# Optimization experiments

Measured on AMD Instinct MI355X. Metric: run time of the kernel, lower is better.

## Reference

```python
import jax, jax.numpy as jnp
import numpy as np

N = 100000   # nodes
K = 32       # fixed neighbor count per node
IN_C = 128
OUT_C = 64


def setup_inputs() -> dict:
    key = jax.random.key(0)
    k1, k2, k3 = jax.random.split(key, 3)
    x = jax.random.normal(k1, (N, IN_C), dtype=jnp.float32)
    nbrs = jax.random.randint(k2, (N, K), 0, N, dtype=jnp.int64)
    # nn.Linear weight [out, in], no bias
    W = jax.random.normal(k3, (OUT_C, IN_C), dtype=jnp.float32) * (1.0 / np.sqrt(IN_C))
    return {"x": x, "nbrs": nbrs, "W": W}


def reference(x, nbrs, W):
    # h = self.w(x): [N, out]
    h = jnp.einsum("ni,oi->no", x, W)
    # gather neighbor features: [N, K, out]
    gathered = h[nbrs]
    # torch.median(dim=0): lower middle element of sorted values (no averaging)
    med_idx = (K - 1) // 2
    out = jnp.sort(gathered, axis=1)[:, med_idx, :]  # [N, out]
    return out
```

## Files before the change

kernel.cpp:

```cpp
#include <hip/hip_runtime.h>
#include <hip/hip_fp16.h>

#define NNODES 100000
#define KNBR 32
#define IN_C 128
#define OUT_C 64

__global__ __launch_bounds__(256) void gemm_h_kernel(
    const float* __restrict__ x, const float* __restrict__ W,
    __half* __restrict__ h)
{
    __shared__ __align__(16) float sx[64 * 68];
    __shared__ __align__(16) float sw[64 * 68];

    const int t = threadIdx.x;
    const int node0 = blockIdx.x * 64;
    const int tx = t & 15;
    const int ty = t >> 4;
    const int kq = t & 15;
    const int sl = t >> 4;

    float acc[4][4];
#pragma unroll
    for (int i = 0; i < 4; ++i)
#pragma unroll
        for (int j = 0; j < 4; ++j) acc[i][j] = 0.f;

    for (int kc = 0; kc < 2; ++kc) {
        const int kbase = kc * 64;
        __syncthreads();
#pragma unroll
        for (int pass = 0; pass < 4; ++pass) {
            const int nl = sl + pass * 16;
            int nn = node0 + nl;
            if (nn > NNODES - 1) nn = NNODES - 1;
            const float4 xv = *(const float4*)(x + nn * IN_C + kbase + 4 * kq);
            sx[(4 * kq + 0) * 68 + nl] = xv.x;
            sx[(4 * kq + 1) * 68 + nl] = xv.y;
            sx[(4 * kq + 2) * 68 + nl] = xv.z;
            sx[(4 * kq + 3) * 68 + nl] = xv.w;
            const float4 wv = *(const float4*)(W + nl * IN_C + kbase + 4 * kq);
            sw[(4 * kq + 0) * 68 + nl] = wv.x;
            sw[(4 * kq + 1) * 68 + nl] = wv.y;
            sw[(4 * kq + 2) * 68 + nl] = wv.z;
            sw[(4 * kq + 3) * 68 + nl] = wv.w;
        }
        __syncthreads();
#pragma unroll 8
        for (int kk = 0; kk < 64; ++kk) {
            const float4 wv = *(const float4*)&sw[kk * 68 + 4 * tx];
            const float4 xv = *(const float4*)&sx[kk * 68 + 4 * ty];
            acc[0][0] += xv.x * wv.x; acc[0][1] += xv.x * wv.y;
            acc[0][2] += xv.x * wv.z; acc[0][3] += xv.x * wv.w;
            acc[1][0] += xv.y * wv.x; acc[1][1] += xv.y * wv.y;
            acc[1][2] += xv.y * wv.z; acc[1][3] += xv.y * wv.w;
            acc[2][0] += xv.z * wv.x; acc[2][1] += xv.z * wv.y;
            acc[2][2] += xv.z * wv.z; acc[2][3] += xv.z * wv.w;
            acc[3][0] += xv.w * wv.x; acc[3][1] += xv.w * wv.y;
            acc[3][2] += xv.w * wv.z; acc[3][3] += xv.w * wv.w;
        }
    }
#pragma unroll
    for (int i = 0; i < 4; ++i) {
        const int node = node0 + 4 * ty + i;
        if (node < NNODES) {
            __half2 p0 = __floats2half2_rn(acc[i][0], acc[i][1]);
            __half2 p1 = __floats2half2_rn(acc[i][2], acc[i][3]);
            uint2 st;
            st.x = *(unsigned int*)&p0;
            st.y = *(unsigned int*)&p1;
            *(uint2*)(h + node * OUT_C + 4 * tx) = st;
        }
    }
}

__device__ __forceinline__ unsigned pk_min(unsigned a, unsigned b) {
    unsigned d;
    asm("v_pk_min_f16 %0, %1, %2" : "=v"(d) : "v"(a), "v"(b));
    return d;
}
__device__ __forceinline__ unsigned pk_max(unsigned a, unsigned b) {
    unsigned d;
    asm("v_pk_max_f16 %0, %1, %2" : "=v"(d) : "v"(a), "v"(b));
    return d;
}
__device__ __forceinline__ void ce(unsigned& a, unsigned& b) {
    const unsigned lo = pk_min(a, b);
    b = pk_max(a, b);
    a = lo;
}

__device__ __forceinline__ void sort16(unsigned* v) {
    constexpr unsigned char net[63][2] = {
        {0,1},{2,3},{4,5},{6,7},{8,9},{10,11},{12,13},{14,15},
        {0,2},{1,3},{4,6},{5,7},{8,10},{9,11},{12,14},{13,15},
        {1,2},{5,6},{9,10},{13,14},
        {0,4},{1,5},{2,6},{3,7},{8,12},{9,13},{10,14},{11,15},
        {2,4},{3,5},{10,12},{11,13},
        {1,2},{3,4},{5,6},{9,10},{11,12},{13,14},
        {0,8},{1,9},{2,10},{3,11},{4,12},{5,13},{6,14},{7,15},
        {4,8},{5,9},{6,10},{7,11},
        {2,4},{3,5},{6,8},{7,9},{10,12},{11,13},
        {1,2},{3,4},{5,6},{7,8},{9,10},{11,12},{13,14}
    };
#pragma unroll
    for (int i = 0; i < 63; ++i) ce(v[net[i][0]], v[net[i][1]]);
}

__device__ __forceinline__ unsigned median32(unsigned* v) {
    sort16(v);
    sort16(v + 16);
    const unsigned* A = v;
    const unsigned* B = v + 16;
    const unsigned e2a = pk_max(pk_max(A[0], B[0]), pk_min(A[8],  B[8]));
    const unsigned o1a = pk_min(pk_max(A[4], B[4]), pk_min(A[12], B[12]));
    const unsigned Ep4 = pk_max(e2a, o1a);
    const unsigned e2b = pk_max(pk_max(A[2], B[2]), pk_min(A[10], B[10]));
    const unsigned o1b = pk_min(pk_max(A[6], B[6]), pk_min(A[14], B[14]));
    const unsigned Op3 = pk_min(e2b, o1b);
    const unsigned E8  = pk_max(Ep4, Op3);
    const unsigned e2c = pk_max(pk_max(A[1], B[1]), pk_min(A[9],  B[9]));
    const unsigned o1c = pk_min(pk_max(A[5], B[5]), pk_min(A[13], B[13]));
    const unsigned Ep4o = pk_max(e2c, o1c);
    const unsigned e2d = pk_max(pk_max(A[3], B[3]), pk_min(A[11], B[11]));
    const unsigned o1d = pk_min(pk_max(A[7], B[7]), pk_min(A[15], B[15]));
    const unsigned Op3o = pk_min(e2d, o1d);
    const unsigned O7  = pk_min(Ep4o, Op3o);
    return pk_min(E8, O7);
}

__global__ __launch_bounds__(256) void median_kernel(
    const __half* __restrict__ h, const int* __restrict__ nbrs,
    float* __restrict__ out)
{
    const int t = threadIdx.x;
    const int li = t & 15;
    const int node = blockIdx.x * 16 + (t >> 4);
    const int ch0 = 4 * li;

    const int ia = nbrs[node * KNBR + li];
    const int ib = nbrs[node * KNBR + 16 + li];

    unsigned a[KNBR];
    unsigned b[KNBR];
#pragma unroll
    for (int k = 0; k < KNBR; ++k) {
        const int row = (k < 16) ? __shfl(ia, k, 16) : __shfl(ib, k - 16, 16);
        const uint2 rv = *(const uint2*)(h + row * OUT_C + ch0);
        a[k] = rv.x;
        b[k] = rv.y;
    }

    const unsigned ma = median32(a);
    const unsigned mb = median32(b);
    const __half2 ha = *(const __half2*)&ma;
    const __half2 hb = *(const __half2*)&mb;

    float4 o;
    o.x = __low2float(ha);
    o.y = __high2float(ha);
    o.z = __low2float(hb);
    o.w = __high2float(hb);
    *(float4*)(out + node * OUT_C + ch0) = o;
}

extern "C" void kernel_launch(void* const* d_in, const int* in_sizes, int n_in,
                              void* d_out, int out_size, void* d_ws, size_t ws_size,
                              hipStream_t stream) {
    (void)in_sizes; (void)n_in; (void)out_size; (void)ws_size;
    const float* x    = (const float*)d_in[0];
    const int*   nbrs = (const int*)d_in[1];
    const float* W    = (const float*)d_in[2];
    float* out = (float*)d_out;
    __half* h  = (__half*)d_ws;

    gemm_h_kernel<<<(NNODES + 63) / 64, 256, 0, stream>>>(x, W, h);
    median_kernel<<<NNODES / 16, 256, 0, stream>>>(h, nbrs, out);
}
```

Baseline: 163.4 us.

## Use split-bf16 MFMA for projection GEMM and halve per-thread median width

```diff
diff --git a/kernel.cpp b/kernel.cpp
--- a/kernel.cpp
+++ b/kernel.cpp
@@ -6,70 +6,110 @@
 #define IN_C 128
 #define OUT_C 64
 
+
+typedef __attribute__((ext_vector_type(8))) short bf16x8;
+typedef __attribute__((ext_vector_type(4))) float f32x4;
+
+__device__ __forceinline__ unsigned short bf16_rne(float f) {
+    unsigned u = __builtin_bit_cast(unsigned, f);
+    u = (u + 0x7FFFu + ((u >> 16) & 1u)) >> 16;
+    return (unsigned short)u;
+}
+__device__ __forceinline__ float bf16_f(unsigned short s) {
+    unsigned u = ((unsigned)s) << 16;
+    return __builtin_bit_cast(float, u);
+}
+
+__device__ __forceinline__ void split8(const float4& u, const float4& v,
+                                       bf16x8& hi, bf16x8& lo) {
+    const float f[8] = {u.x, u.y, u.z, u.w, v.x, v.y, v.z, v.w};
+#pragma unroll
+    for (int j = 0; j < 8; ++j) {
+        const unsigned short hb = bf16_rne(f[j]);
+        hi[j] = (short)hb;
+        lo[j] = (short)bf16_rne(f[j] - bf16_f(hb));
+    }
+}
+
+#define GW_LD 136
+
 __global__ __launch_bounds__(256) void gemm_h_kernel(
     const float* __restrict__ x, const float* __restrict__ W,
     __half* __restrict__ h)
 {
-    __shared__ __align__(16) float sx[64 * 68];
-    __shared__ __align__(16) float sw[64 * 68];
+    __shared__ __align__(16) unsigned short swh[64 * GW_LD];
+    __shared__ __align__(16) unsigned short swl[64 * GW_LD];
 
     const int t = threadIdx.x;
-    const int node0 = blockIdx.x * 64;
-    const int tx = t & 15;
-    const int ty = t >> 4;
-    const int kq = t & 15;
-    const int sl = t >> 4;
-
-    float acc[4][4];
-#pragma unroll
-    for (int i = 0; i < 4; ++i)
-#pragma unroll
-        for (int j = 0; j < 4; ++j) acc[i][j] = 0.f;
-
-    for (int kc = 0; kc < 2; ++kc) {
-        const int kbase = kc * 64;
-        __syncthreads();
-#pragma unroll
-        for (int pass = 0; pass < 4; ++pass) {
-            const int nl = sl + pass * 16;
-            int nn = node0 + nl;
-            if (nn > NNODES - 1) nn = NNODES - 1;
-            const float4 xv = *(const float4*)(x + nn * IN_C + kbase + 4 * kq);
-            sx[(4 * kq + 0) * 68 + nl] = xv.x;
-            sx[(4 * kq + 1) * 68 + nl] = xv.y;
-            sx[(4 * kq + 2) * 68 + nl] = xv.z;
-            sx[(4 * kq + 3) * 68 + nl] = xv.w;
-            const float4 wv = *(const float4*)(W + nl * IN_C + kbase + 4 * kq);
-            sw[(4 * kq + 0) * 68 + nl] = wv.x;
-            sw[(4 * kq + 1) * 68 + nl] = wv.y;
-            sw[(4 * kq + 2) * 68 + nl] = wv.z;
-            sw[(4 * kq + 3) * 68 + nl] = wv.w;
+
+#pragma unroll
+    for (int i = 0; i < 8; ++i) {
+        const int e   = t + 256 * i;
+        const int row = e >> 5;
+        const int c4  = (e & 31) * 4;
+        const float4 wv = *(const float4*)(W + row * IN_C + c4);
+        ushort4 ph, pl;
+        ph.x = bf16_rne(wv.x); pl.x = bf16_rne(wv.x - bf16_f(ph.x));
+        ph.y = bf16_rne(wv.y); pl.y = bf16_rne(wv.y - bf16_f(ph.y));
+        ph.z = bf16_rne(wv.z); pl.z = bf16_rne(wv.z - bf16_f(ph.z));
+        ph.w = bf16_rne(wv.w); pl.w = bf16_rne(wv.w - bf16_f(ph.w));
+        *(ushort4*)(swh + row * GW_LD + c4) = ph;
+        *(ushort4*)(swl + row * GW_LD + c4) = pl;
+    }
+    __syncthreads();
+
+    const int lane = t & 63;
+    const int w    = t >> 6;
+    const int r    = lane & 15;
+    const int g    = lane >> 4;
+    const int nb   = blockIdx.x * 128 + 32 * w;
+
+    f32x4 acc[2][4];
+#pragma unroll
+    for (int i = 0; i < 2; ++i)
+#pragma unroll
+        for (int c = 0; c < 4; ++c) acc[i][c] = (f32x4){0.f, 0.f, 0.f, 0.f};
+
+    int n0 = nb + r;       if (n0 > NNODES - 1) n0 = NNODES - 1;
+    int n1 = nb + 16 + r;  if (n1 > NNODES - 1) n1 = NNODES - 1;
+    const float* px0 = x + (size_t)n0 * IN_C;
+    const float* px1 = x + (size_t)n1 * IN_C;
+
+#pragma unroll
+    for (int ks = 0; ks < 4; ++ks) {
+        const int k0 = 32 * ks + 8 * g;
+        const float4 u0 = *(const float4*)(px0 + k0);
+        const float4 v0 = *(const float4*)(px0 + k0 + 4);
+        const float4 u1 = *(const float4*)(px1 + k0);
+        const float4 v1 = *(const float4*)(px1 + k0 + 4);
+        bf16x8 a0h, a0l, a1h, a1l;
+        split8(u0, v0, a0h, a0l);
+        split8(u1, v1, a1h, a1l);
+#pragma unroll
+        for (int c = 0; c < 4; ++c) {
+            const int wrow = 16 * c + r;
+            const bf16x8 bh = *(const bf16x8*)(swh + wrow * GW_LD + k0);
+            const bf16x8 bl = *(const bf16x8*)(swl + wrow * GW_LD + k0);
+            acc[0][c] = __builtin_amdgcn_mfma_f32_16x16x32_bf16(a0h, bh, acc[0][c], 0, 0, 0);
+            acc[1][c] = __builtin_amdgcn_mfma_f32_16x16x32_bf16(a1h, bh, acc[1][c], 0, 0, 0);
+            acc[0][c] = __builtin_amdgcn_mfma_f32_16x16x32_bf16(a0l, bh, acc[0][c], 0, 0, 0);
+            acc[1][c] = __builtin_amdgcn_mfma_f32_16x16x32_bf16(a1l, bh, acc[1][c], 0, 0, 0);
+            acc[0][c] = __builtin_amdgcn_mfma_f32_16x16x32_bf16(a0h, bl, acc[0][c], 0, 0, 0);
+            acc[1][c] = __builtin_amdgcn_mfma_f32_16x16x32_bf16(a1h, bl, acc[1][c], 0, 0, 0);
         }
-        __syncthreads();
-#pragma unroll 8
-        for (int kk = 0; kk < 64; ++kk) {
-            const float4 wv = *(const float4*)&sw[kk * 68 + 4 * tx];
-            const float4 xv = *(const float4*)&sx[kk * 68 + 4 * ty];
-            acc[0][0] += xv.x * wv.x; acc[0][1] += xv.x * wv.y;
-            acc[0][2] += xv.x * wv.z; acc[0][3] += xv.x * wv.w;
-            acc[1][0] += xv.y * wv.x; acc[1][1] += xv.y * wv.y;
-            acc[1][2] += xv.y * wv.z; acc[1][3] += xv.y * wv.w;
-            acc[2][0] += xv.z * wv.x; acc[2][1] += xv.z * wv.y;
-            acc[2][2] += xv.z * wv.z; acc[2][3] += xv.z * wv.w;
-            acc[3][0] += xv.w * wv.x; acc[3][1] += xv.w * wv.y;
-            acc[3][2] += xv.w * wv.z; acc[3][3] += xv.w * wv.w;
-        }
-    }
-#pragma unroll
-    for (int i = 0; i < 4; ++i) {
-        const int node = node0 + 4 * ty + i;
-        if (node < NNODES) {
-            __half2 p0 = __floats2half2_rn(acc[i][0], acc[i][1]);
-            __half2 p1 = __floats2half2_rn(acc[i][2], acc[i][3]);
-            uint2 st;
-            st.x = *(unsigned int*)&p0;
-            st.y = *(unsigned int*)&p1;
-            *(uint2*)(h + node * OUT_C + 4 * tx) = st;
+    }
+
+#pragma unroll
+    for (int rf = 0; rf < 2; ++rf) {
+#pragma unroll
+        for (int i = 0; i < 4; ++i) {
+            const int node = nb + 16 * rf + 4 * g + i;
+            if (node < NNODES) {
+                __half* ph = h + (size_t)node * OUT_C + r;
+#pragma unroll
+                for (int c = 0; c < 4; ++c)
+                    ph[16 * c] = __float2half(acc[rf][c][i]);
+            }
         }
     }
 }
@@ -134,34 +174,25 @@
     float* __restrict__ out)
 {
     const int t = threadIdx.x;
-    const int li = t & 15;
-    const int node = blockIdx.x * 16 + (t >> 4);
-    const int ch0 = 4 * li;
-
-    const int ia = nbrs[node * KNBR + li];
-    const int ib = nbrs[node * KNBR + 16 + li];
+    const int li   = t & 31;
+    const int node = blockIdx.x * 8 + (t >> 5);
+    const int ch0  = 2 * li;
+
+    const int idx = nbrs[node * KNBR + li];
 
     unsigned a[KNBR];
-    unsigned b[KNBR];
 #pragma unroll
     for (int k = 0; k < KNBR; ++k) {
-        const int row = (k < 16) ? __shfl(ia, k, 16) : __shfl(ib, k - 16, 16);
-        const uint2 rv = *(const uint2*)(h + row * OUT_C + ch0);
-        a[k] = rv.x;
-        b[k] = rv.y;
-    }
-
-    const unsigned ma = median32(a);
-    const unsigned mb = median32(b);
-    const __half2 ha = *(const __half2*)&ma;
-    const __half2 hb = *(const __half2*)&mb;
-
-    float4 o;
-    o.x = __low2float(ha);
-    o.y = __high2float(ha);
-    o.z = __low2float(hb);
-    o.w = __high2float(hb);
-    *(float4*)(out + node * OUT_C + ch0) = o;
+        const int row = __shfl(idx, k, 32);
+        a[k] = *(const unsigned*)(h + row * OUT_C + ch0);
+    }
+
+    const unsigned m = median32(a);
+    const __half2 hm = *(const __half2*)&m;
+    float2 o;
+    o.x = __low2float(hm);
+    o.y = __high2float(hm);
+    *(float2*)(out + node * OUT_C + ch0) = o;
 }
 
 extern "C" void kernel_launch(void* const* d_in, const int* in_sizes, int n_in,
@@ -174,6 +205,6 @@
     float* out = (float*)d_out;
     __half* h  = (__half*)d_ws;
 
-    gemm_h_kernel<<<(NNODES + 63) / 64, 256, 0, stream>>>(x, W, h);
-    median_kernel<<<NNODES / 16, 256, 0, stream>>>(h, nbrs, out);
-}
+    gemm_h_kernel<<<(NNODES + 127) / 128, 256, 0, stream>>>(x, W, h);
+    median_kernel<<<NNODES / 8, 256, 0, stream>>>(h, nbrs, out);
+}
```

Result: faster. 146.6 us (-10.3%).
